# Kernel optimization log

Measured on AMD Instinct MI355X. Metric: run time of the kernel, lower is better.

The kernel has to match this reference:

```python
import jax, jax.numpy as jnp
import numpy as np

# --- hyperparameters (match module defaults) ---
W_CLASSIFY = 1.1          # weight_factor_classify
W_SAMPLE = 1.0            # weight_factor_sample (mid weight add)
LOSS_WEIGHTS = (1.0, 1.0, 1.0)
PARAMS_HEAD = dict(a=80.0, b=1500.0, c=1750.0, d=2000.0, t=-0.5)
PARAMS_CHEST = dict(a=10.0, b=75.0, c=85.0, d=100.0, t=-0.5)
PARAMS_NECK = dict(a=0.15, b=1.5, c=1.7, d=1.9, t=-0.5)

# AIS thresholds (reimplemented in-kernel; original used numpy round-trips)
HEAD_THR = np.array([150.0, 500.0, 1000.0, 1800.0, 2600.0], dtype=np.float32)
CHEST_THR = np.array([22.0, 35.0, 45.0, 55.0, 65.0], dtype=np.float32)
CHEST_OT_SCALE = np.array([0.8, 0.9, 1.0, 1.1, 1.2], dtype=np.float32)  # per occupant-type
NECK_THR = np.array([0.2, 0.5, 1.0, 1.5, 2.0], dtype=np.float32)


def piecewise_linear(y_true, y_pred, p, mid):
    a, b, c, d, t = p['a'], p['b'], p['c'], p['d'], p['t']
    k = -np.log(t + 1.0) / d  # decay rate for y > d
    w = jnp.zeros_like(y_true)
    w = jnp.where((y_true >= 0) & (y_true < a), (mid / a) * y_true, w)
    w = jnp.where((y_true >= a) & (y_true <= b), mid, w)
    w = jnp.where((y_true > b) & (y_true < c), mid - (mid / (c - b)) * (y_true - b), w)
    w = jnp.where((y_true >= c) & (y_true <= d), 0.0, w)
    w = jnp.where(y_true > d, -1.0 + jnp.exp(-k * (y_true - d)), w)
    w = w + jnp.where(y_pred < 0, mid, 0.0)
    return w


def ais_from_thresholds(x, thr):
    # piecewise-constant AIS class: number of thresholds exceeded, in [0, 5]
    return jnp.sum(x[:, None] >= thr[None, :], axis=-1).astype(jnp.float32)


def task_loss(pred, true, ais_pred, ais_true, params):
    # AIS values are classification results of detached values in the
    # original (no grad) -> stop_gradient here.
    w_cls = W_CLASSIFY ** jnp.abs(jax.lax.stop_gradient(ais_pred) - jax.lax.stop_gradient(ais_true))
    w_mid = 1.0 + piecewise_linear(true, pred, params, W_SAMPLE)
    base = jnp.abs(pred - true)  # MAE, reduction='none'
    return jnp.mean(base * w_cls * w_mid)


def setup_inputs() -> dict:
    key = jax.random.key(0)
    k1, k2, k3 = jax.random.split(key, 3)
    B = 4194304
    scales = jnp.array([2500.0, 120.0, 2.5], dtype=jnp.float32)  # HIC, Dmax, Nij ranges
    pred = (jax.random.uniform(k1, (B, 3), dtype=jnp.float32) * 1.1 - 0.05) * scales
    true = jax.random.uniform(k2, (B, 3), dtype=jnp.float32) * scales
    ot = jax.random.randint(k3, (B,), 0, 5, dtype=jnp.int32)
    return {"pred": pred, "true": true, "ot": ot}


def reference(pred, true, ot):
    thr_head = jnp.asarray(HEAD_THR)
    thr_neck = jnp.asarray(NECK_THR)
    # chest thresholds scale with occupant type -> per-sample thresholds
    thr_chest = jnp.asarray(CHEST_THR)[None, :] * jnp.asarray(CHEST_OT_SCALE)[ot][:, None]

    p_hic, p_dmax, p_nij = pred[:, 0], pred[:, 1], pred[:, 2]
    t_hic, t_dmax, t_nij = true[:, 0], true[:, 1], true[:, 2]

    loss_hic = task_loss(p_hic, t_hic,
                         ais_from_thresholds(p_hic, thr_head),
                         ais_from_thresholds(t_hic, thr_head), PARAMS_HEAD)

    ais_p_chest = jnp.sum(p_dmax[:, None] >= thr_chest, axis=-1).astype(jnp.float32)
    ais_t_chest = jnp.sum(t_dmax[:, None] >= thr_chest, axis=-1).astype(jnp.float32)
    loss_dmax = task_loss(p_dmax, t_dmax, ais_p_chest, ais_t_chest, PARAMS_CHEST)

    loss_nij = task_loss(p_nij, t_nij,
                         ais_from_thresholds(p_nij, thr_neck),
                         ais_from_thresholds(t_nij, thr_neck), PARAMS_NECK)

    w_hic, w_dmax, w_nij = LOSS_WEIGHTS
    return w_hic * loss_hic + w_dmax * loss_dmax + w_nij * loss_nij
```

## Files before the change

### kernel.cpp

```cpp
#include <hip/hip_runtime.h>

#define NBLOCKS 1024
#define NTHREADS 256

__device__ __forceinline__ float wmid(float yt, float yp,
                                      float a, float b, float c, float d) {
    float w;
    if (yt < 0.0f)       w = 0.0f;
    else if (yt < a)     w = yt * (1.0f / a);
    else if (yt <= b)    w = 1.0f;
    else if (yt < c)     w = 1.0f - (yt - b) * (1.0f / (c - b));
    else if (yt <= d)    w = 0.0f;
    else                 w = -1.0f + exp2f(-(yt - d) * (1.0f / d));
    if (yp < 0.0f) w += 1.0f;
    return 1.0f + w;
}

__device__ __forceinline__ float row_loss(float ph, float pd, float pn,
                                          float th, float td, float tn, int ot) {
    const float L2_11 = 0.13750352374993502f;

    int ap = (ph >= 150.0f) + (ph >= 500.0f) + (ph >= 1000.0f) + (ph >= 1800.0f) + (ph >= 2600.0f);
    int at = (th >= 150.0f) + (th >= 500.0f) + (th >= 1000.0f) + (th >= 1800.0f) + (th >= 2600.0f);
    float wc = exp2f(fabsf((float)(ap - at)) * L2_11);
    float l  = fabsf(ph - th) * wc * wmid(th, ph, 80.0f, 1500.0f, 1750.0f, 2000.0f);

    float s = 0.8f + 0.1f * (float)ot;
    ap = (pd >= 22.0f*s) + (pd >= 35.0f*s) + (pd >= 45.0f*s) + (pd >= 55.0f*s) + (pd >= 65.0f*s);
    at = (td >= 22.0f*s) + (td >= 35.0f*s) + (td >= 45.0f*s) + (td >= 55.0f*s) + (td >= 65.0f*s);
    wc = exp2f(fabsf((float)(ap - at)) * L2_11);
    l += fabsf(pd - td) * wc * wmid(td, pd, 10.0f, 75.0f, 85.0f, 100.0f);

    ap = (pn >= 0.2f) + (pn >= 0.5f) + (pn >= 1.0f) + (pn >= 1.5f) + (pn >= 2.0f);
    at = (tn >= 0.2f) + (tn >= 0.5f) + (tn >= 1.0f) + (tn >= 1.5f) + (tn >= 2.0f);
    wc = exp2f(fabsf((float)(ap - at)) * L2_11);
    l += fabsf(pn - tn) * wc * wmid(tn, pn, 0.15f, 1.5f, 1.7f, 1.9f);

    return l;
}

__global__ __launch_bounds__(NTHREADS)
void weighted_loss_main(const float* __restrict__ pred,
                        const float* __restrict__ truth,
                        const int*   __restrict__ ot,
                        float* __restrict__ partial, int B) {
    const int nq     = B >> 2;
    const int gid    = blockIdx.x * blockDim.x + threadIdx.x;
    const int stride = gridDim.x * blockDim.x;
    const float4* p4 = (const float4*)pred;
    const float4* t4 = (const float4*)truth;
    const int4*   o4 = (const int4*)ot;

    float acc = 0.0f;
    for (int q = gid; q < nq; q += stride) {
        float4 pa = p4[3*q + 0], pb = p4[3*q + 1], pc = p4[3*q + 2];
        float4 ta = t4[3*q + 0], tb = t4[3*q + 1], tc = t4[3*q + 2];
        int4   o  = o4[q];
        float ph[4] = {pa.x, pa.w, pb.z, pc.y};
        float pD[4] = {pa.y, pb.x, pb.w, pc.z};
        float pn[4] = {pa.z, pb.y, pc.x, pc.w};
        float th[4] = {ta.x, ta.w, tb.z, tc.y};
        float tD[4] = {ta.y, tb.x, tb.w, tc.z};
        float tn[4] = {ta.z, tb.y, tc.x, tc.w};
        int   oo[4] = {o.x, o.y, o.z, o.w};
        #pragma unroll
        for (int j = 0; j < 4; ++j)
            acc += row_loss(ph[j], pD[j], pn[j], th[j], tD[j], tn[j], oo[j]);
    }
    for (int r = (nq << 2) + gid; r < B; r += stride)
        acc += row_loss(pred[3*r], pred[3*r+1], pred[3*r+2],
                        truth[3*r], truth[3*r+1], truth[3*r+2], ot[r]);

    #pragma unroll
    for (int off = 32; off > 0; off >>= 1) acc += __shfl_down(acc, off, 64);
    __shared__ float sm[NTHREADS / 64];
    const int lane = threadIdx.x & 63, wid = threadIdx.x >> 6;
    if (lane == 0) sm[wid] = acc;
    __syncthreads();
    if (threadIdx.x == 0) {
        float s = 0.0f;
        #pragma unroll
        for (int w = 0; w < NTHREADS / 64; ++w) s += sm[w];
        partial[blockIdx.x] = s;
    }
}

__global__ __launch_bounds__(256)
void weighted_loss_reduce(const float* __restrict__ partial, int n,
                          float* __restrict__ out, float invB) {
    float acc = 0.0f;
    for (int i = threadIdx.x; i < n; i += blockDim.x) acc += partial[i];
    #pragma unroll
    for (int off = 32; off > 0; off >>= 1) acc += __shfl_down(acc, off, 64);
    __shared__ float sm[4];
    const int lane = threadIdx.x & 63, wid = threadIdx.x >> 6;
    if (lane == 0) sm[wid] = acc;
    __syncthreads();
    if (threadIdx.x == 0)
        out[0] = (sm[0] + sm[1] + sm[2] + sm[3]) * invB;
}

extern "C" void kernel_launch(void* const* d_in, const int* in_sizes, int n_in,
                              void* d_out, int out_size, void* d_ws, size_t ws_size,
                              hipStream_t stream) {
    const float* pred  = (const float*)d_in[0];
    const float* truth = (const float*)d_in[1];
    const int*   ot    = (const int*)d_in[2];
    const int B = in_sizes[2];
    float* partial = (float*)d_ws;

    weighted_loss_main<<<NBLOCKS, NTHREADS, 0, stream>>>(pred, truth, ot, partial, B);
    weighted_loss_reduce<<<1, 256, 0, stream>>>(partial, NBLOCKS, (float*)d_out,
                                                1.0f / (float)B);
}
```

Baseline: 143.4 us.

## Use branchless clamp weights, hoisted batched loads, and larger grid

Replaces the branchy piecewise weight with a branchless min/max clamp plus an exp2 tail, and scales the chest value by a reciprocal instead of scaling each threshold. Raises the grid to 2048 blocks and adds a fast path for when the work is exactly two quads per thread: all loads are issued up front behind a sched_barrier, then both quads are computed. The reduce kernel grows to 1024 threads. The aim is more memory-level parallelism and fewer divergent branches in a bandwidth-bound reduction. Using a reciprocal multiply for the chest thresholds can flip comparisons right at the boundaries.

```diff
diff --git a/kernel.cpp b/kernel.cpp
--- a/kernel.cpp
+++ b/kernel.cpp
@@ -1,103 +1,129 @@
 #include <hip/hip_runtime.h>
 
-#define NBLOCKS 1024
-#define NTHREADS 256
+#define NT 256
+#define NB 2048
 
-__device__ __forceinline__ float wmid(float yt, float yp,
-                                      float a, float b, float c, float d) {
-    float w;
-    if (yt < 0.0f)       w = 0.0f;
-    else if (yt < a)     w = yt * (1.0f / a);
-    else if (yt <= b)    w = 1.0f;
-    else if (yt < c)     w = 1.0f - (yt - b) * (1.0f / (c - b));
-    else if (yt <= d)    w = 0.0f;
-    else                 w = -1.0f + exp2f(-(yt - d) * (1.0f / d));
-    if (yp < 0.0f) w += 1.0f;
-    return 1.0f + w;
+
+__device__ __forceinline__ float loss_head(float p, float t) {
+    int ap = (p>=150.0f)+(p>=500.0f)+(p>=1000.0f)+(p>=1800.0f)+(p>=2600.0f);
+    int at = (t>=150.0f)+(t>=500.0f)+(t>=1000.0f)+(t>=1800.0f)+(t>=2600.0f);
+    float wc = exp2f(fabsf((float)(ap-at)) * 0.13750352374993502f);
+    float wm = fmaxf(fminf(fminf(t*0.0125f, 1.0f), fmaf(t,-0.004f,7.0f)), 0.0f);
+    float tail = exp2f(fmaf(t,-0.0005f,1.0f)) - 1.0f;
+    wm = (t>2000.0f) ? tail : wm;
+    wm += (p<0.0f) ? 2.0f : 1.0f;
+    return fabsf(p-t)*wc*wm;
 }
 
-__device__ __forceinline__ float row_loss(float ph, float pd, float pn,
-                                          float th, float td, float tn, int ot) {
-    const float L2_11 = 0.13750352374993502f;
-
-    int ap = (ph >= 150.0f) + (ph >= 500.0f) + (ph >= 1000.0f) + (ph >= 1800.0f) + (ph >= 2600.0f);
-    int at = (th >= 150.0f) + (th >= 500.0f) + (th >= 1000.0f) + (th >= 1800.0f) + (th >= 2600.0f);
-    float wc = exp2f(fabsf((float)(ap - at)) * L2_11);
-    float l  = fabsf(ph - th) * wc * wmid(th, ph, 80.0f, 1500.0f, 1750.0f, 2000.0f);
-
-    float s = 0.8f + 0.1f * (float)ot;
-    ap = (pd >= 22.0f*s) + (pd >= 35.0f*s) + (pd >= 45.0f*s) + (pd >= 55.0f*s) + (pd >= 65.0f*s);
-    at = (td >= 22.0f*s) + (td >= 35.0f*s) + (td >= 45.0f*s) + (td >= 55.0f*s) + (td >= 65.0f*s);
-    wc = exp2f(fabsf((float)(ap - at)) * L2_11);
-    l += fabsf(pd - td) * wc * wmid(td, pd, 10.0f, 75.0f, 85.0f, 100.0f);
-
-    ap = (pn >= 0.2f) + (pn >= 0.5f) + (pn >= 1.0f) + (pn >= 1.5f) + (pn >= 2.0f);
-    at = (tn >= 0.2f) + (tn >= 0.5f) + (tn >= 1.0f) + (tn >= 1.5f) + (tn >= 2.0f);
-    wc = exp2f(fabsf((float)(ap - at)) * L2_11);
-    l += fabsf(pn - tn) * wc * wmid(tn, pn, 0.15f, 1.5f, 1.7f, 1.9f);
-
-    return l;
+__device__ __forceinline__ float loss_chest(float p, float t, float rs) {
+    float ps = p*rs, ts = t*rs;
+    int ap = (ps>=22.0f)+(ps>=35.0f)+(ps>=45.0f)+(ps>=55.0f)+(ps>=65.0f);
+    int at = (ts>=22.0f)+(ts>=35.0f)+(ts>=45.0f)+(ts>=55.0f)+(ts>=65.0f);
+    float wc = exp2f(fabsf((float)(ap-at)) * 0.13750352374993502f);
+    float wm = fmaxf(fminf(fminf(t*0.1f, 1.0f), fmaf(t,-0.1f,8.5f)), 0.0f);
+    float tail = exp2f(fmaf(t,-0.01f,1.0f)) - 1.0f;
+    wm = (t>100.0f) ? tail : wm;
+    wm += (p<0.0f) ? 2.0f : 1.0f;
+    return fabsf(p-t)*wc*wm;
 }
 
-__global__ __launch_bounds__(NTHREADS)
+__device__ __forceinline__ float loss_neck(float p, float t) {
+    int ap = (p>=0.2f)+(p>=0.5f)+(p>=1.0f)+(p>=1.5f)+(p>=2.0f);
+    int at = (t>=0.2f)+(t>=0.5f)+(t>=1.0f)+(t>=1.5f)+(t>=2.0f);
+    float wc = exp2f(fabsf((float)(ap-at)) * 0.13750352374993502f);
+    float wm = fmaxf(fminf(fminf(t*6.6666667f, 1.0f), fmaf(t,-5.0f,8.5f)), 0.0f);
+    float tail = exp2f(fmaf(t,-0.52631579f,1.0f)) - 1.0f;
+    wm = (t>1.9f) ? tail : wm;
+    wm += (p<0.0f) ? 2.0f : 1.0f;
+    return fabsf(p-t)*wc*wm;
+}
+
+__device__ __forceinline__ float quad_loss(float4 p0, float4 p1, float4 p2,
+                                           float4 t0, float4 t1, float4 t2,
+                                           int4 o) {
+    float r0 = __builtin_amdgcn_rcpf(fmaf(0.1f,(float)o.x,0.8f));
+    float r1 = __builtin_amdgcn_rcpf(fmaf(0.1f,(float)o.y,0.8f));
+    float r2 = __builtin_amdgcn_rcpf(fmaf(0.1f,(float)o.z,0.8f));
+    float r3 = __builtin_amdgcn_rcpf(fmaf(0.1f,(float)o.w,0.8f));
+    float a;
+    a  = loss_head (p0.x,t0.x) + loss_chest(p0.y,t0.y,r0) + loss_neck(p0.z,t0.z);
+    a += loss_head (p0.w,t0.w) + loss_chest(p1.x,t1.x,r1) + loss_neck(p1.y,t1.y);
+    a += loss_head (p1.z,t1.z) + loss_chest(p1.w,t1.w,r2) + loss_neck(p2.x,t2.x);
+    a += loss_head (p2.y,t2.y) + loss_chest(p2.z,t2.z,r3) + loss_neck(p2.w,t2.w);
+    return a;
+}
+
+__global__ __launch_bounds__(NT)
 void weighted_loss_main(const float* __restrict__ pred,
                         const float* __restrict__ truth,
                         const int*   __restrict__ ot,
                         float* __restrict__ partial, int B) {
-    const int nq     = B >> 2;
-    const int gid    = blockIdx.x * blockDim.x + threadIdx.x;
-    const int stride = gridDim.x * blockDim.x;
+    const int nquad = B >> 2;
+    const int g = blockIdx.x * NT + threadIdx.x;
+    const int T = gridDim.x * NT;
     const float4* p4 = (const float4*)pred;
     const float4* t4 = (const float4*)truth;
     const int4*   o4 = (const int4*)ot;
 
     float acc = 0.0f;
-    for (int q = gid; q < nq; q += stride) {
-        float4 pa = p4[3*q + 0], pb = p4[3*q + 1], pc = p4[3*q + 2];
-        float4 ta = t4[3*q + 0], tb = t4[3*q + 1], tc = t4[3*q + 2];
-        int4   o  = o4[q];
-        float ph[4] = {pa.x, pa.w, pb.z, pc.y};
-        float pD[4] = {pa.y, pb.x, pb.w, pc.z};
-        float pn[4] = {pa.z, pb.y, pc.x, pc.w};
-        float th[4] = {ta.x, ta.w, tb.z, tc.y};
-        float tD[4] = {ta.y, tb.x, tb.w, tc.z};
-        float tn[4] = {ta.z, tb.y, tc.x, tc.w};
-        int   oo[4] = {o.x, o.y, o.z, o.w};
-        #pragma unroll
-        for (int j = 0; j < 4; ++j)
-            acc += row_loss(ph[j], pD[j], pn[j], th[j], tD[j], tn[j], oo[j]);
+
+    if (nquad == 2*T) {
+        const int qa = g, qb = g + T;
+        float4 pa0=p4[3*qa], pa1=p4[3*qa+1], pa2=p4[3*qa+2];
+        float4 ta0=t4[3*qa], ta1=t4[3*qa+1], ta2=t4[3*qa+2];
+        int4   oa = o4[qa];
+        float4 pb0=p4[3*qb], pb1=p4[3*qb+1], pb2=p4[3*qb+2];
+        float4 tb0=t4[3*qb], tb1=t4[3*qb+1], tb2=t4[3*qb+2];
+        int4   ob = o4[qb];
+        __builtin_amdgcn_sched_barrier(0);
+        acc += quad_loss(pa0,pa1,pa2, ta0,ta1,ta2, oa);
+        acc += quad_loss(pb0,pb1,pb2, tb0,tb1,tb2, ob);
+    } else {
+        for (int q = g; q < nquad; q += T) {
+            float4 p0=p4[3*q], p1=p4[3*q+1], p2=p4[3*q+2];
+            float4 t0=t4[3*q], t1=t4[3*q+1], t2=t4[3*q+2];
+            int4 o = o4[q];
+            acc += quad_loss(p0,p1,p2, t0,t1,t2, o);
+        }
+        for (int r = (nquad<<2) + g; r < B; r += T) {
+            float rs = __builtin_amdgcn_rcpf(fmaf(0.1f,(float)ot[r],0.8f));
+            acc += loss_head (pred[3*r],   truth[3*r])
+                 + loss_chest(pred[3*r+1], truth[3*r+1], rs)
+                 + loss_neck (pred[3*r+2], truth[3*r+2]);
+        }
     }
-    for (int r = (nq << 2) + gid; r < B; r += stride)
-        acc += row_loss(pred[3*r], pred[3*r+1], pred[3*r+2],
-                        truth[3*r], truth[3*r+1], truth[3*r+2], ot[r]);
 
     #pragma unroll
     for (int off = 32; off > 0; off >>= 1) acc += __shfl_down(acc, off, 64);
-    __shared__ float sm[NTHREADS / 64];
+    __shared__ float sm[NT / 64];
     const int lane = threadIdx.x & 63, wid = threadIdx.x >> 6;
     if (lane == 0) sm[wid] = acc;
     __syncthreads();
     if (threadIdx.x == 0) {
         float s = 0.0f;
         #pragma unroll
-        for (int w = 0; w < NTHREADS / 64; ++w) s += sm[w];
+        for (int w = 0; w < NT / 64; ++w) s += sm[w];
         partial[blockIdx.x] = s;
     }
 }
 
-__global__ __launch_bounds__(256)
+__global__ __launch_bounds__(1024)
 void weighted_loss_reduce(const float* __restrict__ partial, int n,
                           float* __restrict__ out, float invB) {
     float acc = 0.0f;
     for (int i = threadIdx.x; i < n; i += blockDim.x) acc += partial[i];
     #pragma unroll
     for (int off = 32; off > 0; off >>= 1) acc += __shfl_down(acc, off, 64);
-    __shared__ float sm[4];
+    __shared__ float sm[16];
     const int lane = threadIdx.x & 63, wid = threadIdx.x >> 6;
     if (lane == 0) sm[wid] = acc;
     __syncthreads();
-    if (threadIdx.x == 0)
-        out[0] = (sm[0] + sm[1] + sm[2] + sm[3]) * invB;
+    if (threadIdx.x == 0) {
+        float s = 0.0f;
+        #pragma unroll
+        for (int w = 0; w < 16; ++w) s += sm[w];
+        out[0] = s * invB;
+    }
 }
 
 extern "C" void kernel_launch(void* const* d_in, const int* in_sizes, int n_in,
@@ -109,7 +135,7 @@
     const int B = in_sizes[2];
     float* partial = (float*)d_ws;
 
-    weighted_loss_main<<<NBLOCKS, NTHREADS, 0, stream>>>(pred, truth, ot, partial, B);
-    weighted_loss_reduce<<<1, 256, 0, stream>>>(partial, NBLOCKS, (float*)d_out,
-                                                1.0f / (float)B);
+    weighted_loss_main<<<NB, NT, 0, stream>>>(pred, truth, ot, partial, B);
+    weighted_loss_reduce<<<1, 1024, 0, stream>>>(partial, NB, (float*)d_out,
+                                                 1.0f / (float)B);
 }
```

Measured after the change: 141.0 us. Within noise of the previous version (-1.6%).
